# Kernel optimization log

Measured on AMD Instinct MI355X. Metric: run time of the kernel, lower is better.

Reference implementation:

```python
import jax, jax.numpy as jnp
import numpy as np

N, H, P, L, E, F = 131072, 256, 32768, 16, 8, 16
FUSED = 3 * H + E + F  # 792


def setup_inputs() -> dict:
    key = jax.random.key(0)
    ks = jax.random.split(key, 8)
    return {
        "node_embs": jax.random.normal(ks[0], (N, H), jnp.float32),
        "path_nodes": jax.random.randint(ks[1], (P, L), 0, N),
        "path_lens": jax.random.randint(ks[2], (P,), 0, L + 1),
        "path_edge_feats": jax.random.normal(ks[3], (P, E), jnp.float32),
        "path_scalar_feats": jax.random.normal(ks[4], (P, F), jnp.float32),
        "W1": jax.random.normal(ks[5], (FUSED, H), jnp.float32) / np.float32(np.sqrt(FUSED)),
        "b1": jnp.zeros((H,), jnp.float32),
        "W2": jax.random.normal(ks[6], (H, 1), jnp.float32) / np.float32(np.sqrt(H)),
        "b2": jnp.zeros((1,), jnp.float32),
        "src_idx": 0,
        "dst_idx": 1,
    }


def reference(node_embs, path_nodes, path_lens, path_edge_feats, path_scalar_feats,
              W1, b1, W2, b2, src_idx, dst_idx):
    dt = node_embs.dtype
    # ragged per-path mean over node embeddings, padded to [P, L]
    mask = (jnp.arange(L)[None, :] < path_lens[:, None]).astype(dt)  # [P, L]
    gathered = node_embs[path_nodes]                                  # [P, L, H]
    denom = jnp.maximum(path_lens, 1).astype(dt)[:, None]             # [P, 1]
    path_emb = jnp.einsum('plh,pl->ph', gathered, mask) / denom       # [P, H]

    src = jnp.broadcast_to(node_embs[src_idx], (P, H))
    dst = jnp.broadcast_to(node_embs[dst_idx], (P, H))
    fused = jnp.concatenate([src, dst, path_emb, path_edge_feats, path_scalar_feats], axis=1)  # [P, FUSED]

    h = jax.nn.relu(fused @ W1 + b1)   # [P, H]
    q = (h @ W2 + b2)[:, 0]            # [P]
    # empty paths produce exactly 0.0, matching the torch branch
    return jnp.where(path_lens > 0, q, jnp.zeros((), dt))
```

## Files before the change

### kernel.cpp

```cpp
#include <hip/hip_runtime.h>

#define NN      131072
#define H       256
#define PPATHS  32768
#define LMAX    16
#define EF      8
#define FF      16
#define KP      288
#define GB      (PPATHS/4)

typedef short v8s __attribute__((ext_vector_type(8)));
typedef float v4f __attribute__((ext_vector_type(4)));

__device__ __forceinline__ unsigned short f2bf(float x) {
    unsigned int u = __float_as_uint(x);
    u += 0x7fffu + ((u >> 16) & 1u);
    return (unsigned short)(u >> 16);
}

__global__ __launch_bounds__(256) void gather_prep_kernel(
        const float* __restrict__ node_embs,
        const int*   __restrict__ path_nodes,
        const int*   __restrict__ path_lens,
        const float* __restrict__ edge_f,
        const float* __restrict__ scal_f,
        const float* __restrict__ W1,
        const float* __restrict__ b1,
        const int*   __restrict__ si,
        const int*   __restrict__ di,
        unsigned short* __restrict__ feat,
        unsigned short* __restrict__ W1T,
        float*       __restrict__ cvec) {
    __shared__ float red[256];
    const int bid = blockIdx.x;

    if (bid >= GB) {
        const int b = bid - GB;
        if (b < KP) {
            const int k = b, n = threadIdx.x;
            float v = 0.0f;
            if (k < 256)      v = W1[(size_t)(512 + k) * H + n];
            else if (k < 280) v = W1[(size_t)(768 + (k - 256)) * H + n];
            W1T[(size_t)n * KP + k] = f2bf(v);
        } else {
            const int jb = b - KP;
            const int t  = threadIdx.x;
            const int jl = t & 3, kp = t >> 2;
            const int j  = jb * 4 + jl;
            const float* src = node_embs + (size_t)si[0] * H;
            const float* dst = node_embs + (size_t)di[0] * H;
            float c = 0.0f;
            #pragma unroll
            for (int i = 0; i < 8; ++i) {
                int k = kp + i * 64;
                float f = (k < H) ? src[k] : dst[k - H];
                c += f * W1[(size_t)k * H + j];
            }
            red[t] = c;
            __syncthreads();
            for (int s = 128; s >= 4; s >>= 1) {
                if (t < s) red[t] += red[t + s];
                __syncthreads();
            }
            if (t < 4) cvec[jb * 4 + t] = b1[jb * 4 + t] + red[t];
        }
        return;
    }

    const int wave = threadIdx.x >> 6, lane = threadIdx.x & 63;
    const int p    = bid * 4 + wave;
    const int len  = path_lens[p];
    const int iv   = path_nodes[(size_t)p * LMAX + (lane & 15)];

    float4 a0 = make_float4(0, 0, 0, 0), a1 = make_float4(0, 0, 0, 0);
    float4 a2 = make_float4(0, 0, 0, 0), a3 = make_float4(0, 0, 0, 0);
    int l = 0;
    for (; l + 3 < len; l += 4) {
        const int n0 = __shfl(iv, l);
        const int n1 = __shfl(iv, l + 1);
        const int n2 = __shfl(iv, l + 2);
        const int n3 = __shfl(iv, l + 3);
        const float4 v0 = ((const float4*)(node_embs + (size_t)n0 * H))[lane];
        const float4 v1 = ((const float4*)(node_embs + (size_t)n1 * H))[lane];
        const float4 v2 = ((const float4*)(node_embs + (size_t)n2 * H))[lane];
        const float4 v3 = ((const float4*)(node_embs + (size_t)n3 * H))[lane];
        a0.x += v0.x; a0.y += v0.y; a0.z += v0.z; a0.w += v0.w;
        a1.x += v1.x; a1.y += v1.y; a1.z += v1.z; a1.w += v1.w;
        a2.x += v2.x; a2.y += v2.y; a2.z += v2.z; a2.w += v2.w;
        a3.x += v3.x; a3.y += v3.y; a3.z += v3.z; a3.w += v3.w;
    }
    for (; l < len; ++l) {
        const int n0 = __shfl(iv, l);
        const float4 v0 = ((const float4*)(node_embs + (size_t)n0 * H))[lane];
        a0.x += v0.x; a0.y += v0.y; a0.z += v0.z; a0.w += v0.w;
    }
    const float inv = 1.0f / (float)max(len, 1);
    ushort4 r;
    r.x = f2bf((a0.x + a1.x + a2.x + a3.x) * inv);
    r.y = f2bf((a0.y + a1.y + a2.y + a3.y) * inv);
    r.z = f2bf((a0.z + a1.z + a2.z + a3.z) * inv);
    r.w = f2bf((a0.w + a1.w + a2.w + a3.w) * inv);
    *(ushort4*)(feat + (size_t)p * KP + 4 * lane) = r;

    if (lane < 32) {
        float v = 0.0f;
        if (lane < EF)            v = edge_f[(size_t)p * EF + lane];
        else if (lane < EF + FF)  v = scal_f[(size_t)p * FF + (lane - EF)];
        feat[(size_t)p * KP + H + lane] = f2bf(v);
    }
}

__global__ __launch_bounds__(256) void gemm_kernel(
        const unsigned short* __restrict__ feat,
        const unsigned short* __restrict__ W1T,
        const float* __restrict__ cvec,
        const float* __restrict__ W2,
        const float* __restrict__ b2,
        const int*   __restrict__ path_lens,
        float*       __restrict__ out) {
    __shared__ float qpart[32][5];
    const int wave = threadIdx.x >> 6, lane = threadIdx.x & 63;
    const int pb   = blockIdx.x * 32;
    const int col  = lane & 15, quad = lane >> 4;
    const int n0   = wave * 64;

    v4f acc[2][4];
    float w2v[4];
    #pragma unroll
    for (int nt = 0; nt < 4; ++nt) {
        const float cv = cvec[n0 + nt * 16 + col];
        w2v[nt] = W2[n0 + nt * 16 + col];
        #pragma unroll
        for (int mt = 0; mt < 2; ++mt)
            acc[mt][nt] = (v4f){cv, cv, cv, cv};
    }

    const unsigned short* Abase = feat + (size_t)(pb + col) * KP + quad * 8;
    const unsigned short* Bbase = W1T + (size_t)(n0 + col) * KP + quad * 8;

    for (int k0 = 0; k0 < KP; k0 += 32) {
        v8s a[2], b[4];
        #pragma unroll
        for (int mt = 0; mt < 2; ++mt)
            a[mt] = *(const v8s*)(Abase + (size_t)(mt * 16) * KP + k0);
        #pragma unroll
        for (int nt = 0; nt < 4; ++nt)
            b[nt] = *(const v8s*)(Bbase + (size_t)(nt * 16) * KP + k0);
        #pragma unroll
        for (int mt = 0; mt < 2; ++mt)
            #pragma unroll
            for (int nt = 0; nt < 4; ++nt)
                acc[mt][nt] = __builtin_amdgcn_mfma_f32_16x16x32_bf16(
                                  a[mt], b[nt], acc[mt][nt], 0, 0, 0);
    }

    #pragma unroll
    for (int mt = 0; mt < 2; ++mt) {
        float s[4];
        #pragma unroll
        for (int r = 0; r < 4; ++r) {
            float v = 0.0f;
            #pragma unroll
            for (int nt = 0; nt < 4; ++nt)
                v += fmaxf(acc[mt][nt][r], 0.0f) * w2v[nt];
            s[r] = v;
        }
        #pragma unroll
        for (int off = 1; off < 16; off <<= 1) {
            #pragma unroll
            for (int r = 0; r < 4; ++r)
                s[r] += __shfl_xor(s[r], off);
        }
        if (col == 0) {
            #pragma unroll
            for (int r = 0; r < 4; ++r)
                qpart[mt * 16 + quad * 4 + r][wave] = s[r];
        }
    }
    __syncthreads();

    if (threadIdx.x < 32) {
        const int t = threadIdx.x;
        const float q = qpart[t][0] + qpart[t][1] + qpart[t][2] + qpart[t][3] + b2[0];
        out[pb + t] = (path_lens[pb + t] > 0) ? q : 0.0f;
    }
}

extern "C" void kernel_launch(void* const* d_in, const int* in_sizes, int n_in,
                              void* d_out, int out_size, void* d_ws, size_t ws_size,
                              hipStream_t stream) {
    const float* node_embs  = (const float*)d_in[0];
    const int*   path_nodes = (const int*)d_in[1];
    const int*   path_lens  = (const int*)d_in[2];
    const float* edge_f     = (const float*)d_in[3];
    const float* scal_f     = (const float*)d_in[4];
    const float* W1         = (const float*)d_in[5];
    const float* b1         = (const float*)d_in[6];
    const float* W2         = (const float*)d_in[7];
    const float* b2         = (const float*)d_in[8];
    const int*   si         = (const int*)d_in[9];
    const int*   di         = (const int*)d_in[10];
    float* out = (float*)d_out;

    float*          cvec = (float*)d_ws;
    unsigned short* W1T  = (unsigned short*)((char*)d_ws + 1024);
    unsigned short* feat = (unsigned short*)((char*)d_ws + 148480);

    hipLaunchKernelGGL(gather_prep_kernel, dim3(GB + KP + 64), dim3(256), 0, stream,
                       node_embs, path_nodes, path_lens, edge_f, scal_f,
                       W1, b1, si, di, feat, W1T, cvec);
    hipLaunchKernelGGL(gemm_kernel, dim3(PPATHS / 32), dim3(256), 0, stream,
                       feat, W1T, cvec, W2, b2, path_lens, out);
}
```

Measured before the change: 234.1 us.

## Fuse path gather into GEMM kernel via shared-memory feature tile

Moves the ragged per-path mean gather into the MFMA GEMM kernel. Each block builds its 32-path bf16 feature tile in LDS (padded row stride 296) instead of writing it to and reading it back from global workspace. Weight transpose and the constant src/dst vector move to a small separate prep kernel. This removes the global round-trip of the feature matrix, but each block now does the gather (8 paths per wave, serial) before the GEMM, and the whole block waits at the barrier before the GEMM starts.

```diff
diff --git a/kernel.cpp b/kernel.cpp
--- a/kernel.cpp
+++ b/kernel.cpp
@@ -7,7 +7,8 @@
 #define EF      8
 #define FF      16
 #define KP      288
-#define GB      (PPATHS/4)
+#define TPB     32
+#define FS      296
 
 typedef short v8s __attribute__((ext_vector_type(8)));
 typedef float v4f __attribute__((ext_vector_type(4)));
@@ -18,111 +19,112 @@
     return (unsigned short)(u >> 16);
 }
 
-__global__ __launch_bounds__(256) void gather_prep_kernel(
+__global__ __launch_bounds__(256) void prep_kernel(
+        const float* __restrict__ node_embs,
+        const float* __restrict__ W1,
+        const float* __restrict__ b1,
+        const int*   __restrict__ si,
+        const int*   __restrict__ di,
+        unsigned short* __restrict__ W1T,
+        float*       __restrict__ cvec) {
+    __shared__ float red[256];
+    const int b = blockIdx.x;
+    if (b < KP) {
+        const int k = b, n = threadIdx.x;
+        float v = 0.0f;
+        if (k < 256)      v = W1[(size_t)(512 + k) * H + n];
+        else if (k < 280) v = W1[(size_t)(768 + (k - 256)) * H + n];
+        W1T[(size_t)n * KP + k] = f2bf(v);
+    } else {
+        const int jb = b - KP;
+        const int t  = threadIdx.x;
+        const int jl = t & 3, kp = t >> 2;
+        const int j  = jb * 4 + jl;
+        const float* src = node_embs + (size_t)si[0] * H;
+        const float* dst = node_embs + (size_t)di[0] * H;
+        float c = 0.0f;
+        #pragma unroll
+        for (int i = 0; i < 8; ++i) {
+            int k = kp + i * 64;
+            float f = (k < H) ? src[k] : dst[k - H];
+            c += f * W1[(size_t)k * H + j];
+        }
+        red[t] = c;
+        __syncthreads();
+        for (int s = 128; s >= 4; s >>= 1) {
+            if (t < s) red[t] += red[t + s];
+            __syncthreads();
+        }
+        if (t < 4) cvec[jb * 4 + t] = b1[jb * 4 + t] + red[t];
+    }
+}
+
+__global__ __launch_bounds__(256, 4) void fused_kernel(
         const float* __restrict__ node_embs,
         const int*   __restrict__ path_nodes,
         const int*   __restrict__ path_lens,
         const float* __restrict__ edge_f,
         const float* __restrict__ scal_f,
-        const float* __restrict__ W1,
-        const float* __restrict__ b1,
-        const int*   __restrict__ si,
-        const int*   __restrict__ di,
-        unsigned short* __restrict__ feat,
-        unsigned short* __restrict__ W1T,
-        float*       __restrict__ cvec) {
-    __shared__ float red[256];
-    const int bid = blockIdx.x;
-
-    if (bid >= GB) {
-        const int b = bid - GB;
-        if (b < KP) {
-            const int k = b, n = threadIdx.x;
-            float v = 0.0f;
-            if (k < 256)      v = W1[(size_t)(512 + k) * H + n];
-            else if (k < 280) v = W1[(size_t)(768 + (k - 256)) * H + n];
-            W1T[(size_t)n * KP + k] = f2bf(v);
-        } else {
-            const int jb = b - KP;
-            const int t  = threadIdx.x;
-            const int jl = t & 3, kp = t >> 2;
-            const int j  = jb * 4 + jl;
-            const float* src = node_embs + (size_t)si[0] * H;
-            const float* dst = node_embs + (size_t)di[0] * H;
-            float c = 0.0f;
-            #pragma unroll
-            for (int i = 0; i < 8; ++i) {
-                int k = kp + i * 64;
-                float f = (k < H) ? src[k] : dst[k - H];
-                c += f * W1[(size_t)k * H + j];
-            }
-            red[t] = c;
-            __syncthreads();
-            for (int s = 128; s >= 4; s >>= 1) {
-                if (t < s) red[t] += red[t + s];
-                __syncthreads();
-            }
-            if (t < 4) cvec[jb * 4 + t] = b1[jb * 4 + t] + red[t];
-        }
-        return;
-    }
-
-    const int wave = threadIdx.x >> 6, lane = threadIdx.x & 63;
-    const int p    = bid * 4 + wave;
-    const int len  = path_lens[p];
-    const int iv   = path_nodes[(size_t)p * LMAX + (lane & 15)];
-
-    float4 a0 = make_float4(0, 0, 0, 0), a1 = make_float4(0, 0, 0, 0);
-    float4 a2 = make_float4(0, 0, 0, 0), a3 = make_float4(0, 0, 0, 0);
-    int l = 0;
-    for (; l + 3 < len; l += 4) {
-        const int n0 = __shfl(iv, l);
-        const int n1 = __shfl(iv, l + 1);
-        const int n2 = __shfl(iv, l + 2);
-        const int n3 = __shfl(iv, l + 3);
-        const float4 v0 = ((const float4*)(node_embs + (size_t)n0 * H))[lane];
-        const float4 v1 = ((const float4*)(node_embs + (size_t)n1 * H))[lane];
-        const float4 v2 = ((const float4*)(node_embs + (size_t)n2 * H))[lane];
-        const float4 v3 = ((const float4*)(node_embs + (size_t)n3 * H))[lane];
-        a0.x += v0.x; a0.y += v0.y; a0.z += v0.z; a0.w += v0.w;
-        a1.x += v1.x; a1.y += v1.y; a1.z += v1.z; a1.w += v1.w;
-        a2.x += v2.x; a2.y += v2.y; a2.z += v2.z; a2.w += v2.w;
-        a3.x += v3.x; a3.y += v3.y; a3.z += v3.z; a3.w += v3.w;
-    }
-    for (; l < len; ++l) {
-        const int n0 = __shfl(iv, l);
-        const float4 v0 = ((const float4*)(node_embs + (size_t)n0 * H))[lane];
-        a0.x += v0.x; a0.y += v0.y; a0.z += v0.z; a0.w += v0.w;
-    }
-    const float inv = 1.0f / (float)max(len, 1);
-    ushort4 r;
-    r.x = f2bf((a0.x + a1.x + a2.x + a3.x) * inv);
-    r.y = f2bf((a0.y + a1.y + a2.y + a3.y) * inv);
-    r.z = f2bf((a0.z + a1.z + a2.z + a3.z) * inv);
-    r.w = f2bf((a0.w + a1.w + a2.w + a3.w) * inv);
-    *(ushort4*)(feat + (size_t)p * KP + 4 * lane) = r;
-
-    if (lane < 32) {
-        float v = 0.0f;
-        if (lane < EF)            v = edge_f[(size_t)p * EF + lane];
-        else if (lane < EF + FF)  v = scal_f[(size_t)p * FF + (lane - EF)];
-        feat[(size_t)p * KP + H + lane] = f2bf(v);
-    }
-}
-
-__global__ __launch_bounds__(256) void gemm_kernel(
-        const unsigned short* __restrict__ feat,
         const unsigned short* __restrict__ W1T,
         const float* __restrict__ cvec,
         const float* __restrict__ W2,
         const float* __restrict__ b2,
-        const int*   __restrict__ path_lens,
         float*       __restrict__ out) {
-    __shared__ float qpart[32][5];
-    const int wave = threadIdx.x >> 6, lane = threadIdx.x & 63;
-    const int pb   = blockIdx.x * 32;
-    const int col  = lane & 15, quad = lane >> 4;
-    const int n0   = wave * 64;
+    __shared__ __align__(16) unsigned short feat[TPB * FS];
+    __shared__ float qpart[TPB][5];
+
+    const int tid  = threadIdx.x;
+    const int wave = tid >> 6, lane = tid & 63;
+    const int pb   = blockIdx.x * TPB;
+
+    for (int i = tid; i < TPB * 32; i += 256) {
+        const int p = i >> 5, s = i & 31;
+        float v = 0.0f;
+        if (s < EF)           v = edge_f[(size_t)(pb + p) * EF + s];
+        else if (s < EF + FF) v = scal_f[(size_t)(pb + p) * FF + (s - EF)];
+        feat[p * FS + H + s] = f2bf(v);
+    }
+
+    for (int pi = 0; pi < 8; ++pi) {
+        const int p   = wave * 8 + pi;
+        const int gp  = pb + p;
+        const int len = path_lens[gp];
+        const int iv  = path_nodes[(size_t)gp * LMAX + (lane & 15)];
+
+        float4 a0 = make_float4(0, 0, 0, 0), a1 = make_float4(0, 0, 0, 0);
+        float4 a2 = make_float4(0, 0, 0, 0), a3 = make_float4(0, 0, 0, 0);
+        int l = 0;
+        for (; l + 3 < len; l += 4) {
+            const int n0 = __shfl(iv, l);
+            const int n1 = __shfl(iv, l + 1);
+            const int n2 = __shfl(iv, l + 2);
+            const int n3 = __shfl(iv, l + 3);
+            const float4 v0 = ((const float4*)(node_embs + (size_t)n0 * H))[lane];
+            const float4 v1 = ((const float4*)(node_embs + (size_t)n1 * H))[lane];
+            const float4 v2 = ((const float4*)(node_embs + (size_t)n2 * H))[lane];
+            const float4 v3 = ((const float4*)(node_embs + (size_t)n3 * H))[lane];
+            a0.x += v0.x; a0.y += v0.y; a0.z += v0.z; a0.w += v0.w;
+            a1.x += v1.x; a1.y += v1.y; a1.z += v1.z; a1.w += v1.w;
+            a2.x += v2.x; a2.y += v2.y; a2.z += v2.z; a2.w += v2.w;
+            a3.x += v3.x; a3.y += v3.y; a3.z += v3.z; a3.w += v3.w;
+        }
+        for (; l < len; ++l) {
+            const int n0 = __shfl(iv, l);
+            const float4 v0 = ((const float4*)(node_embs + (size_t)n0 * H))[lane];
+            a0.x += v0.x; a0.y += v0.y; a0.z += v0.z; a0.w += v0.w;
+        }
+        const float inv = 1.0f / (float)max(len, 1);
+        ushort4 r;
+        r.x = f2bf((a0.x + a1.x + a2.x + a3.x) * inv);
+        r.y = f2bf((a0.y + a1.y + a2.y + a3.y) * inv);
+        r.z = f2bf((a0.z + a1.z + a2.z + a3.z) * inv);
+        r.w = f2bf((a0.w + a1.w + a2.w + a3.w) * inv);
+        *(ushort4*)&feat[p * FS + 4 * lane] = r;
+    }
+    __syncthreads();
+
+    const int col = lane & 15, quad = lane >> 4;
+    const int n0  = wave * 64;
 
     v4f acc[2][4];
     float w2v[4];
@@ -135,14 +137,14 @@
             acc[mt][nt] = (v4f){cv, cv, cv, cv};
     }
 
-    const unsigned short* Abase = feat + (size_t)(pb + col) * KP + quad * 8;
+    const unsigned short* Alds  = feat + col * FS + quad * 8;
     const unsigned short* Bbase = W1T + (size_t)(n0 + col) * KP + quad * 8;
 
     for (int k0 = 0; k0 < KP; k0 += 32) {
         v8s a[2], b[4];
         #pragma unroll
         for (int mt = 0; mt < 2; ++mt)
-            a[mt] = *(const v8s*)(Abase + (size_t)(mt * 16) * KP + k0);
+            a[mt] = *(const v8s*)(Alds + mt * 16 * FS + k0);
         #pragma unroll
         for (int nt = 0; nt < 4; ++nt)
             b[nt] = *(const v8s*)(Bbase + (size_t)(nt * 16) * KP + k0);
@@ -179,10 +181,9 @@
     }
     __syncthreads();
 
-    if (threadIdx.x < 32) {
-        const int t = threadIdx.x;
-        const float q = qpart[t][0] + qpart[t][1] + qpart[t][2] + qpart[t][3] + b2[0];
-        out[pb + t] = (path_lens[pb + t] > 0) ? q : 0.0f;
+    if (tid < TPB) {
+        const float q = qpart[tid][0] + qpart[tid][1] + qpart[tid][2] + qpart[tid][3] + b2[0];
+        out[pb + tid] = (path_lens[pb + tid] > 0) ? q : 0.0f;
     }
 }
 
@@ -204,11 +205,10 @@
 
     float*          cvec = (float*)d_ws;
     unsigned short* W1T  = (unsigned short*)((char*)d_ws + 1024);
-    unsigned short* feat = (unsigned short*)((char*)d_ws + 148480);
-
-    hipLaunchKernelGGL(gather_prep_kernel, dim3(GB + KP + 64), dim3(256), 0, stream,
+
+    hipLaunchKernelGGL(prep_kernel, dim3(KP + 64), dim3(256), 0, stream,
+                       node_embs, W1, b1, si, di, W1T, cvec);
+    hipLaunchKernelGGL(fused_kernel, dim3(PPATHS / TPB), dim3(256), 0, stream,
                        node_embs, path_nodes, path_lens, edge_f, scal_f,
-                       W1, b1, si, di, feat, W1T, cvec);
-    hipLaunchKernelGGL(gemm_kernel, dim3(PPATHS / 32), dim3(256), 0, stream,
-                       feat, W1T, cvec, W2, b2, path_lens, out);
-}
+                       W1T, cvec, W2, b2, out);
+}
```

Measured after the change: 230.1 us. About the same (-1.7%).
